# Optimization experiments

Measured on AMD Instinct MI355X. Metric: run time of the kernel, lower is better.

Reference implementation:

```python
import jax, jax.numpy as jnp
import numpy as np

D_MODEL = 1024
EXPAND = 2
D_INNER = D_MODEL * EXPAND  # 2048
D_STATE = 16
D_CONV = 4
B, T = 4, 2048


def setup_inputs() -> dict:
    key = jax.random.key(0)
    ks = jax.random.split(key, 8)
    s = 0.02  # small init std for numeric stability
    return {
        "x": jax.random.normal(ks[0], (B, T, D_MODEL), jnp.float32),
        "in_proj_w": jax.random.normal(ks[1], (2 * D_INNER, D_MODEL), jnp.float32) * s,
        "conv_w": jax.random.normal(ks[2], (D_INNER, 1, D_CONV), jnp.float32) * s,
        "conv_b": jnp.zeros((D_INNER,), jnp.float32),
        "x_proj_w": jax.random.normal(ks[3], (2 * D_STATE, D_INNER), jnp.float32) * s,
        "dt_proj_w": jax.random.normal(ks[4], (D_INNER, D_STATE), jnp.float32) * s,
        "dt_proj_b": jnp.zeros((D_INNER,), jnp.float32),
        "D_param": jnp.ones((D_INNER,), jnp.float32),
        "out_proj_w": jax.random.normal(ks[5], (D_MODEL, D_INNER), jnp.float32) * s,
    }


def reference(x, in_proj_w, conv_w, conv_b, x_proj_w, dt_proj_w, dt_proj_b, D_param, out_proj_w):
    Bsz, Tlen, _ = x.shape
    # in_proj (no bias), torch Linear: x @ W.T
    xz = jnp.einsum('btd,ed->bte', x, in_proj_w)            # [B,T,2*D_INNER]
    x_inner, z = jnp.split(xz, 2, axis=-1)                   # each [B,T,D_INNER]
    # depthwise causal conv1d: left-pad d_conv-1, take first T outputs
    xc = jnp.transpose(x_inner, (0, 2, 1))                   # [B,D_INNER,T]
    xc = jax.lax.conv_general_dilated(
        xc, conv_w, window_strides=(1,), padding=[(D_CONV - 1, 0)],
        feature_group_count=D_INNER)
    xc = xc + conv_b[None, :, None]
    x_conv = jax.nn.silu(jnp.transpose(xc, (0, 2, 1)))       # [B,T,D_INNER]
    # x_proj -> (B_ssm, C_ssm); C_ssm is unused by the simplified scan (faithful)
    x_ssm = jnp.einsum('btd,ed->bte', x_conv, x_proj_w)      # [B,T,2*D_STATE]
    B_ssm, C_ssm = jnp.split(x_ssm, 2, axis=-1)
    dt = jax.nn.softplus(jnp.einsum('btn,dn->btd', B_ssm, dt_proj_w) + dt_proj_b)  # [B,T,D_INNER]
    # simplified selective scan: EMA with scalar-per-timestep gate
    alpha = jax.nn.sigmoid(jnp.mean(dt, axis=-1, keepdims=True))  # [B,T,1]

    def step(h, inp):
        a, xt = inp
        h = a * h + (1.0 - a) * xt
        return h, h

    aT = jnp.transpose(alpha, (1, 0, 2))   # [T,B,1]
    xT = jnp.transpose(x_conv, (1, 0, 2))  # [T,B,D_INNER]
    h0 = jnp.zeros((Bsz, D_INNER), x.dtype)
    _, ys = jax.lax.scan(step, h0, (aT, xT))
    y = jnp.transpose(ys, (1, 0, 2))        # [B,T,D_INNER]
    y = y * D_param + x_conv                # skip with learned D
    y = y * jax.nn.silu(z)                  # gate
    out = jnp.einsum('btd,ed->bte', y, out_proj_w)  # [B,T,D_MODEL]
    return out
```

## Files before the change

kernel.cpp:

```cpp
#include <hip/hip_runtime.h>
#include <stdint.h>

#define TLEN   2048
#define DMODEL 1024
#define DINNER 2048
#define MROWS  8192
#define NCH    16
#define CHUNK  128

typedef unsigned short u16;
typedef __bf16 bf16x8 __attribute__((ext_vector_type(8)));
typedef float  f32x4  __attribute__((ext_vector_type(4)));

__device__ __forceinline__ float bf2f(u16 u) {
  union { unsigned int i; float f; } v; v.i = ((unsigned int)u) << 16; return v.f;
}
__device__ __forceinline__ u16 f2bf(float f) {
  union { float f; unsigned int u; } v; v.f = f;
  unsigned int u = v.u;
  return (u16)((u + 0x7fffu + ((u >> 16) & 1u)) >> 16);
}
__device__ __forceinline__ float silu_f(float x) { return x / (1.f + __expf(-x)); }

__device__ __forceinline__ void async16(const u16* g, u16* l) {
  __builtin_amdgcn_global_load_lds(
      (const __attribute__((address_space(1))) void*)(g),
      (__attribute__((address_space(3))) void*)(l),
      16, 0, 0);
}

__global__ __launch_bounds__(256) void k_convert(const float* __restrict__ x,
    const float* __restrict__ w1, const float* __restrict__ w3,
    const float* __restrict__ xpw,
    u16* __restrict__ xb, u16* __restrict__ w1b, u16* __restrict__ w3b,
    u16* __restrict__ xpwb) {
  int i = blockIdx.x * 256 + threadIdx.x;
  const int nx  = MROWS * DMODEL / 4;
  const int nw1 = 2 * DINNER * DMODEL / 4;
  const int nw3 = DMODEL * DINNER / 4;
  const float* src; u16* dst; int j;
  if (i < nx)                  { src = x;   dst = xb;   j = i; }
  else if (i < nx + nw1)       { src = w1;  dst = w1b;  j = i - nx; }
  else if (i < nx + nw1 + nw3) { src = w3;  dst = w3b;  j = i - nx - nw1; }
  else                         { src = xpw; dst = xpwb; j = i - nx - nw1 - nw3; }
  float4 v = ((const float4*)src)[j];
  ushort4 o;
  o.x = f2bf(v.x); o.y = f2bf(v.y); o.z = f2bf(v.z); o.w = f2bf(v.w);
  ((ushort4*)dst)[j] = o;
}

template<int N, int K, bool OUT_BF16>
__global__ __launch_bounds__(256) void k_gemm_bt(const u16* __restrict__ A,
    const u16* __restrict__ B, void* __restrict__ C) {
  __shared__ u16 sA[2][128 * 32];
  __shared__ u16 sB[2][128 * 32];
  const int tid  = threadIdx.x;
  const int lane = tid & 63;
  const int wave = tid >> 6;
  const int wm   = (wave >> 1) * 64;
  const int wn   = (wave & 1) * 64;
  const int fr   = lane & 15;
  const int q    = lane >> 4;
  const size_t blockM = (size_t)blockIdx.y * 128;
  const size_t blockN = (size_t)blockIdx.x * 128;

  const int srow = lane >> 2;
  const int scol = (lane & 3) * 8;
  const u16* gA = A + (blockM + (size_t)wave * 32 + srow) * (size_t)K + scol;
  const u16* gB = B + (blockN + (size_t)wave * 32 + srow) * (size_t)K + scol;
  u16* lA0 = sA[0] + wave * 1024;
  u16* lA1 = sA[1] + wave * 1024;
  u16* lB0 = sB[0] + wave * 1024;
  u16* lB1 = sB[1] + wave * 1024;

  f32x4 acc[4][4] = {};

  for (int kt = 0; kt < K; kt += 64) {
    async16(gA + kt,                        lA0);
    async16(gA + 16 * (size_t)K + kt,       lA0 + 512);
    async16(gA + kt + 32,                   lA1);
    async16(gA + 16 * (size_t)K + kt + 32,  lA1 + 512);
    async16(gB + kt,                        lB0);
    async16(gB + 16 * (size_t)K + kt,       lB0 + 512);
    async16(gB + kt + 32,                   lB1);
    async16(gB + 16 * (size_t)K + kt + 32,  lB1 + 512);
    __syncthreads();

    #pragma unroll
    for (int h = 0; h < 2; h++) {
      bf16x8 af[4], bfr[4];
      #pragma unroll
      for (int tm = 0; tm < 4; tm++)
        af[tm] = *(const bf16x8*)(sA[h] + (wm + tm * 16 + fr) * 32 + q * 8);
      #pragma unroll
      for (int tn = 0; tn < 4; tn++)
        bfr[tn] = *(const bf16x8*)(sB[h] + (wn + tn * 16 + fr) * 32 + q * 8);
      #pragma unroll
      for (int tm = 0; tm < 4; tm++)
        #pragma unroll
        for (int tn = 0; tn < 4; tn++)
          acc[tm][tn] = __builtin_amdgcn_mfma_f32_16x16x32_bf16(
              af[tm], bfr[tn], acc[tm][tn], 0, 0, 0);
    }
    __syncthreads();
  }

  #pragma unroll
  for (int tm = 0; tm < 4; tm++)
    #pragma unroll
    for (int tn = 0; tn < 4; tn++)
      #pragma unroll
      for (int r = 0; r < 4; r++) {
        size_t row = blockM + wm + tm * 16 + q * 4 + r;
        size_t col = blockN + wn + tn * 16 + fr;
        float v = acc[tm][tn][r];
        if (OUT_BF16) ((u16*)C)[row * N + col] = f2bf(v);
        else          ((float*)C)[row * N + col] = v;
      }
}

__global__ __launch_bounds__(256) void k_conv(const u16* __restrict__ xz,
    const float* __restrict__ cw, const float* __restrict__ cb,
    u16* __restrict__ xc) {
  int idx = blockIdx.x * 256 + threadIdx.x;
  int d  = idx & (DINNER - 1);
  int tb = (idx >> 11) & 255;
  int b  = idx >> 19;
  float4 w = ((const float4*)cw)[d];
  float bias = cb[d];
  const u16* inp = xz + ((size_t)(b * TLEN + tb * 8)) * 4096 + d;
  float v[11];
  #pragma unroll
  for (int j = 0; j < 11; j++) {
    int t = tb * 8 - 3 + j;
    v[j] = (t >= 0) ? bf2f(inp[(ptrdiff_t)(j - 3) * 4096]) : 0.f;
  }
  u16* outp = xc + ((size_t)(b * TLEN + tb * 8)) * DINNER + d;
  #pragma unroll
  for (int i = 0; i < 8; i++) {
    float acc = bias + w.x * v[i] + w.y * v[i + 1] + w.z * v[i + 2] + w.w * v[i + 3];
    outp[(size_t)i * DINNER] = f2bf(silu_f(acc));
  }
}

__global__ __launch_bounds__(256) void k_bssm(const u16* __restrict__ xc,
    const u16* __restrict__ xpwb, float* __restrict__ bssm) {
  const int tid  = threadIdx.x;
  const int lane = tid & 63;
  const int wave = tid >> 6;
  const int fr   = lane & 15;
  const int q    = lane >> 4;
  const size_t row0 = (size_t)blockIdx.x * 32;
  const int k0 = wave * 512;

  f32x4 acc[2] = {};
  #pragma unroll
  for (int kk = 0; kk < 512; kk += 32) {
    const int kb = k0 + kk + q * 8;
    bf16x8 bfrag = *(const bf16x8*)(xpwb + (size_t)fr * DINNER + kb);
    #pragma unroll
    for (int tm = 0; tm < 2; tm++) {
      bf16x8 afrag = *(const bf16x8*)(xc + (row0 + tm * 16 + fr) * (size_t)DINNER + kb);
      acc[tm] = __builtin_amdgcn_mfma_f32_16x16x32_bf16(afrag, bfrag, acc[tm], 0, 0, 0);
    }
  }

  __shared__ float red[4][32][16];
  #pragma unroll
  for (int tm = 0; tm < 2; tm++)
    #pragma unroll
    for (int r = 0; r < 4; r++)
      red[wave][tm * 16 + q * 4 + r][fr] = acc[tm][r];
  __syncthreads();
  #pragma unroll
  for (int i = tid; i < 512; i += 256) {
    int r = i >> 4, n = i & 15;
    bssm[(row0 + r) * 16 + n] =
        red[0][r][n] + red[1][r][n] + red[2][r][n] + red[3][r][n];
  }
}

__global__ __launch_bounds__(256) void k_alpha(const float* __restrict__ bssm,
    const float* __restrict__ dtw, const float* __restrict__ dtb,
    float* __restrict__ alpha) {
  const int tid = threadIdx.x;
  const size_t row0 = (size_t)blockIdx.x * 16;
  __shared__ float4 sB[16][4];
  { int r = tid >> 4, n = tid & 15;
    ((float*)&sB[r][0])[n] = bssm[(row0 + r) * 16 + n]; }
  __syncthreads();

  float rowsum[16];
  #pragma unroll
  for (int r = 0; r < 16; r++) rowsum[r] = 0.f;

  #pragma unroll 1
  for (int m = 0; m < 4; m++) {
    const int d0 = m * 512 + tid * 2;
    float4 w[2][4]; float bias[2];
    #pragma unroll
    for (int j = 0; j < 2; j++) {
      const float4* wp = (const float4*)(dtw + (size_t)(d0 + j) * 16);
      w[j][0] = wp[0]; w[j][1] = wp[1]; w[j][2] = wp[2]; w[j][3] = wp[3];
      bias[j] = dtb[d0 + j];
    }
    #pragma unroll
    for (int r = 0; r < 16; r++) {
      float4 b0 = sB[r][0], b1 = sB[r][1], b2 = sB[r][2], b3 = sB[r][3];
      float s = 0.f;
      #pragma unroll
      for (int j = 0; j < 2; j++) {
        float dot = bias[j]
          + b0.x * w[j][0].x + b0.y * w[j][0].y + b0.z * w[j][0].z + b0.w * w[j][0].w
          + b1.x * w[j][1].x + b1.y * w[j][1].y + b1.z * w[j][1].z + b1.w * w[j][1].w
          + b2.x * w[j][2].x + b2.y * w[j][2].y + b2.z * w[j][2].z + b2.w * w[j][2].w
          + b3.x * w[j][3].x + b3.y * w[j][3].y + b3.z * w[j][3].z + b3.w * w[j][3].w;
        s += (dot > 15.f) ? dot : __logf(1.f + __expf(dot));
      }
      rowsum[r] += s;
    }
  }
  #pragma unroll
  for (int r = 0; r < 16; r++)
    #pragma unroll
    for (int off = 32; off > 0; off >>= 1) rowsum[r] += __shfl_xor(rowsum[r], off);
  __shared__ float red[4][16];
  if ((tid & 63) == 0) {
    #pragma unroll
    for (int r = 0; r < 16; r++) red[tid >> 6][r] = rowsum[r];
  }
  __syncthreads();
  if (tid < 16) {
    float mean = (red[0][tid] + red[1][tid] + red[2][tid] + red[3][tid]) * (1.f / DINNER);
    alpha[row0 + tid] = 1.f / (1.f + __expf(-mean));
  }
}

__global__ __launch_bounds__(256) void k_scan1(const u16* __restrict__ xc,
    const float* __restrict__ alpha, float* __restrict__ carry) {
  const int blk = blockIdx.x;
  const int g = blk & 7;
  const int c = (blk >> 3) & 15;
  const int b = blk >> 7;
  const int d = g * 256 + threadIdx.x;
  __shared__ float sa[CHUNK];
  if (threadIdx.x < CHUNK) sa[threadIdx.x] = alpha[b * TLEN + c * CHUNK + threadIdx.x];
  __syncthreads();
  const u16* xp = xc + ((size_t)(b * TLEN + c * CHUNK)) * DINNER + d;
  float h = 0.f;
  #pragma unroll 8
  for (int i = 0; i < CHUNK; i++) {
    float a = sa[i];
    float xv = bf2f(xp[(size_t)i * DINNER]);
    h = a * h + (1.f - a) * xv;
  }
  carry[((size_t)(b * NCH + c)) * DINNER + d] = h;
}

__global__ __launch_bounds__(256) void k_scan2(float* __restrict__ carry,
    const float* __restrict__ alpha) {
  int i = blockIdx.x * 256 + threadIdx.x;
  int b = i >> 11;
  int d = i & (DINNER - 1);
  __shared__ float sP[NCH];
  if (threadIdx.x < NCH) {
    const float* ap = alpha + b * TLEN + threadIdx.x * CHUNK;
    float p = 1.f;
    for (int j = 0; j < CHUNK; j++) p *= ap[j];
    sP[threadIdx.x] = p;
  }
  __syncthreads();
  float h = 0.f;
  #pragma unroll
  for (int c = 0; c < NCH; c++) {
    size_t idx = ((size_t)(b * NCH + c)) * DINNER + d;
    float cv = carry[idx];
    carry[idx] = h;
    h = sP[c] * h + cv;
  }
}

__global__ __launch_bounds__(256) void k_scan3(const u16* __restrict__ xc,
    const u16* __restrict__ xz, const float* __restrict__ alpha,
    const float* __restrict__ Hs, const float* __restrict__ Dp,
    u16* __restrict__ yg) {
  const int blk = blockIdx.x;
  const int g = blk & 7;
  const int c = (blk >> 3) & 15;
  const int b = blk >> 7;
  const int d = g * 256 + threadIdx.x;
  __shared__ float sa[CHUNK];
  if (threadIdx.x < CHUNK) sa[threadIdx.x] = alpha[b * TLEN + c * CHUNK + threadIdx.x];
  __syncthreads();
  float h = Hs[((size_t)(b * NCH + c)) * DINNER + d];
  const float Dv = Dp[d];
  const size_t row0 = (size_t)(b * TLEN + c * CHUNK);
  #pragma unroll 4
  for (int i = 0; i < CHUNK; i++) {
    size_t row = row0 + i;
    float a = sa[i];
    float xv = bf2f(xc[row * DINNER + d]);
    h = a * h + (1.f - a) * xv;
    float zv = bf2f(xz[row * 4096 + DINNER + d]);
    float y = h * Dv + xv;
    yg[row * DINNER + d] = f2bf(y * silu_f(zv));
  }
}

extern "C" void kernel_launch(void* const* d_in, const int* in_sizes, int n_in,
                              void* d_out, int out_size, void* d_ws, size_t ws_size,
                              hipStream_t stream) {
  const float* x   = (const float*)d_in[0];
  const float* w1  = (const float*)d_in[1];
  const float* cw  = (const float*)d_in[2];
  const float* cb  = (const float*)d_in[3];
  const float* xpw = (const float*)d_in[4];
  const float* dtw = (const float*)d_in[5];
  const float* dtb = (const float*)d_in[6];
  const float* Dp  = (const float*)d_in[7];
  const float* w3  = (const float*)d_in[8];
  float* out = (float*)d_out;
  char* ws = (char*)d_ws;

  u16*   xb    = (u16*)(ws + 0);
  u16*   w1b   = (u16*)(ws + 16777216);
  u16*   w3b   = (u16*)(ws + 25165824);
  u16*   xz    = (u16*)(ws + 29360128);
  u16*   xc    = (u16*)(ws + 96468992);
  u16*   yg    = (u16*)(ws + 130023424);
  float* bssm  = (float*)(ws + 163577856);
  float* alpha = (float*)(ws + 164102144);
  float* carry = (float*)(ws + 164135168);
  u16*   xpwb  = (u16*)(ws + 164659456);

  k_convert<<<14368, 256, 0, stream>>>(x, w1, w3, xpw, xb, w1b, w3b, xpwb);
  k_gemm_bt<4096, 1024, true ><<<dim3(32, 64), 256, 0, stream>>>(xb, w1b, xz);
  k_conv   <<<8192, 256, 0, stream>>>(xz, cw, cb, xc);
  k_bssm   <<<256, 256, 0, stream>>>(xc, xpwb, bssm);
  k_alpha  <<<512, 256, 0, stream>>>(bssm, dtw, dtb, alpha);
  k_scan1  <<<512, 256, 0, stream>>>(xc, alpha, carry);
  k_scan2  <<<32, 256, 0, stream>>>(carry, alpha);
  k_scan3  <<<512, 256, 0, stream>>>(xc, xz, alpha, carry, Dp, yg);
  k_gemm_bt<1024, 2048, false><<<dim3(8, 64), 256, 0, stream>>>(yg, w3b, out);
}
```

Measured before the change: 327.8 us.

## Replace in_proj GEMM with 256x256 eight-wave ping-pong pipelined MFMA kernel

Adds a new bf16 GEMM kernel with 256x256 tiles, 8 waves, 128KB dynamic LDS, XOR-swizzled async global-to-LDS loads, interleaved staging and MFMA phases separated by barriers with s_setprio, and a grid swizzle for L2 locality. It replaces the 128x128 kernel for the in_proj GEMM (8192x4096x1024). The intent is higher MFMA utilisation through larger tiles and overlapped loads. It risks register pressure with 128 accumulators per thread, barrier overhead, and fewer blocks (512) for the GPU's CUs.

```diff
diff --git a/kernel.cpp b/kernel.cpp
--- a/kernel.cpp
+++ b/kernel.cpp
@@ -28,6 +28,11 @@
       (__attribute__((address_space(3))) void*)(l),
       16, 0, 0);
 }
+
+#define BAR      asm volatile("s_barrier" ::: "memory")
+#define WAITV(n) asm volatile("s_waitcnt vmcnt(" #n ")" ::: "memory")
+#define PRIO1    __builtin_amdgcn_s_setprio(1)
+#define PRIO0    __builtin_amdgcn_s_setprio(0)
 
 __global__ __launch_bounds__(256) void k_convert(const float* __restrict__ x,
     const float* __restrict__ w1, const float* __restrict__ w3,
@@ -49,6 +54,152 @@
   ((ushort4*)dst)[j] = o;
 }
 
+__device__ __forceinline__ u16* regp(u16* lds, int s, int mat, int h) {
+  return lds + (((s * 2 + mat) * 2 + h) * 8192);
+}
+
+__device__ __forceinline__ void read_a(bf16x8 (&dst)[4][2], const u16* reg,
+                                       int qa, int fr, int c0, int c1) {
+  #pragma unroll
+  for (int m = 0; m < 4; m++) {
+    const u16* p = reg + (qa * 64 + m * 16 + fr) * 64;
+    dst[m][0] = *(const bf16x8*)(p + c0);
+    dst[m][1] = *(const bf16x8*)(p + c1);
+  }
+}
+__device__ __forceinline__ void read_b(bf16x8 (&dst)[2][2], const u16* reg,
+                                       int rb, int c0, int c1) {
+  #pragma unroll
+  for (int n = 0; n < 2; n++) {
+    const u16* p = reg + (rb + n * 16) * 64;
+    dst[n][0] = *(const bf16x8*)(p + c0);
+    dst[n][1] = *(const bf16x8*)(p + c1);
+  }
+}
+__device__ __forceinline__ void mfma_quad(f32x4 (&acc)[8][4],
+    const bf16x8 (&af)[4][2], const bf16x8 (&bf)[2][2], int qa, int qb) {
+  #pragma unroll
+  for (int m = 0; m < 4; m++)
+    #pragma unroll
+    for (int n = 0; n < 2; n++)
+      #pragma unroll
+      for (int ks = 0; ks < 2; ks++)
+        acc[qa * 4 + m][qb * 2 + n] = __builtin_amdgcn_mfma_f32_16x16x32_bf16(
+            af[m][ks], bf[n][ks], acc[qa * 4 + m][qb * 2 + n], 0, 0, 0);
+}
+
+template<int N, int K, bool OUT_BF16>
+__global__ __launch_bounds__(512, 2) void k_gemm8p(const u16* __restrict__ A,
+    const u16* __restrict__ Bm, void* __restrict__ C) {
+  static_assert(K % 128 == 0, "K must be multiple of 128");
+  extern __shared__ u16 lds[];
+  const int tid  = threadIdx.x;
+  const int lane = tid & 63;
+  const int wave = tid >> 6;
+  const int wm   = wave >> 2;
+  const int wn   = wave & 3;
+  const int fr   = lane & 15;
+  const int q    = lane >> 4;
+
+  int wg = blockIdx.x, nwg = gridDim.x, swz = wg;
+  if ((nwg & 7) == 0) swz = (wg & 7) * (nwg >> 3) + (wg >> 3);
+  const int NT_N = N / 256;
+  const size_t blockM = (size_t)(swz / NT_N) * 256;
+  const size_t blockN = (size_t)(swz % NT_N) * 256;
+
+  const int rsub   = tid >> 3;
+  const int srcCol = 8 * ((tid & 7) ^ (rsub & 7));
+  const u16* gA = A  + (blockM + rsub) * (size_t)K + srcCol;
+  const u16* gB = Bm + (blockN + rsub) * (size_t)K + srcCol;
+
+#define STAGE(sl, mat, h, kt) do {                                           \
+    const u16* _g = ((mat) ? gB : gA) + (size_t)(h) * (128 * (size_t)K)      \
+                    + (size_t)(kt) * 64;                                     \
+    u16* _l = regp(lds, (sl), (mat), (h)) + tid * 8;                         \
+    async16(_g, _l);                                                         \
+    async16(_g + (size_t)64 * K, _l + 4096);                                 \
+  } while (0)
+
+  const int c0 = (((q * 16)      ^ ((fr & 7) << 4)) >> 1);
+  const int c1 = (((64 + q * 16) ^ ((fr & 7) << 4)) >> 1);
+  const int rb = (wn & 1) * 64 + fr;
+
+  f32x4 acc[8][4] = {};
+  bf16x8 a0[4][2], a1[4][2], bl[2][2], bh[2][2];
+
+  const int NT = K / 64;
+  const int NITER = K / 128;
+
+  STAGE(0, 0, 0, 0); STAGE(0, 0, 1, 0); STAGE(0, 1, 0, 0); STAGE(0, 1, 1, 0);
+  STAGE(1, 1, 0, 1); STAGE(1, 1, 1, 1); STAGE(1, 0, 0, 1);
+  WAITV(6);
+  BAR;
+
+  for (int it = 0; it < NITER; ++it) {
+    const int t2 = 2 * it + 2, t3 = 2 * it + 3;
+    const bool pf = (t2 < NT);
+    read_a(a0, regp(lds, 0, 0, wm), 0, fr, c0, c1);
+    read_b(bl, regp(lds, 0, 1, wn >> 1), rb,      c0, c1);
+    read_b(bh, regp(lds, 0, 1, wn >> 1), rb + 32, c0, c1);
+    STAGE(1, 0, 1, 2 * it + 1);
+    BAR;
+    PRIO1; mfma_quad(acc, a0, bl, 0, 0); PRIO0;
+    BAR;
+    read_a(a1, regp(lds, 0, 0, wm), 1, fr, c0, c1);
+    if (pf) STAGE(0, 1, 0, t2);
+    BAR;
+    PRIO1; mfma_quad(acc, a0, bh, 0, 1); PRIO0;
+    BAR;
+    if (pf) STAGE(0, 1, 1, t2);
+    BAR;
+    PRIO1; mfma_quad(acc, a1, bl, 1, 0); PRIO0;
+    BAR;
+    if (pf) STAGE(0, 0, 0, t2);
+    BAR;
+    PRIO1; mfma_quad(acc, a1, bh, 1, 1); PRIO0;
+    if (pf) { WAITV(6); } else { WAITV(0); }
+    BAR;
+    read_a(a0, regp(lds, 1, 0, wm), 0, fr, c0, c1);
+    read_b(bl, regp(lds, 1, 1, wn >> 1), rb,      c0, c1);
+    read_b(bh, regp(lds, 1, 1, wn >> 1), rb + 32, c0, c1);
+    if (pf) STAGE(0, 0, 1, t2);
+    BAR;
+    PRIO1; mfma_quad(acc, a0, bl, 0, 0); PRIO0;
+    BAR;
+    read_a(a1, regp(lds, 1, 0, wm), 1, fr, c0, c1);
+    if (pf) STAGE(1, 1, 0, t3);
+    BAR;
+    PRIO1; mfma_quad(acc, a0, bh, 0, 1); PRIO0;
+    BAR;
+    if (pf) STAGE(1, 1, 1, t3);
+    BAR;
+    PRIO1; mfma_quad(acc, a1, bl, 1, 0); PRIO0;
+    BAR;
+    if (pf) STAGE(1, 0, 0, t3);
+    BAR;
+    PRIO1; mfma_quad(acc, a1, bh, 1, 1); PRIO0;
+    if (pf) { WAITV(6); BAR; } else { BAR; }
+  }
+#undef STAGE
+
+  {
+    const size_t r0  = blockM + (size_t)wm * 128;
+    const size_t cc0 = blockN + (size_t)wn * 64;
+    #pragma unroll
+    for (int m = 0; m < 8; m++)
+      #pragma unroll
+      for (int n = 0; n < 4; n++)
+        #pragma unroll
+        for (int r = 0; r < 4; r++) {
+          size_t row = r0 + m * 16 + q * 4 + r;
+          size_t col = cc0 + n * 16 + fr;
+          float v = acc[m][n][r];
+          if (OUT_BF16) ((u16*)C)[row * N + col] = f2bf(v);
+          else          ((float*)C)[row * N + col] = v;
+        }
+  }
+}
+
 template<int N, int K, bool OUT_BF16>
 __global__ __launch_bounds__(256) void k_gemm_bt(const u16* __restrict__ A,
     const u16* __restrict__ B, void* __restrict__ C) {
@@ -334,7 +485,7 @@
   u16*   xpwb  = (u16*)(ws + 164659456);
 
   k_convert<<<14368, 256, 0, stream>>>(x, w1, w3, xpw, xb, w1b, w3b, xpwb);
-  k_gemm_bt<4096, 1024, true ><<<dim3(32, 64), 256, 0, stream>>>(xb, w1b, xz);
+  k_gemm8p<4096, 1024, true><<<512, 512, 131072, stream>>>(xb, w1b, xz);
   k_conv   <<<8192, 256, 0, stream>>>(xz, cw, cb, xc);
   k_bssm   <<<256, 256, 0, stream>>>(xc, xpwb, bssm);
   k_alpha  <<<512, 256, 0, stream>>>(bssm, dtw, dtb, alpha);
```

New measurement: 325.6 us. Within noise of the previous version (-0.7%).
